# Kernel optimization log

Measured on AMD Instinct MI355X. Metric: run time of the kernel, lower is better.

The kernel has to match this reference:

```python
import jax, jax.numpy as jnp
import numpy as np

N_RF = 25   # contour integration RF extent (must be odd, 7-55)
N_CH = 96   # AlexNet conv1 feature maps


def _get_coaligned_masks(weights_type, rf_len, non_overlapping_rfs=True):
    """Faithful numpy replication of the manually-defined coalignment masks."""
    half_rf = rf_len // 2
    kernel = np.zeros((N_CH, rf_len, rf_len), dtype=np.float32)
    step = 3 if non_overlapping_rfs else 1
    pre = list(range(0, half_rf, step))
    post = list(range(half_rf + step, rf_len, step))
    kernel[10, pre, half_rf] = 1
    kernel[10, post, half_rf] = 1
    if weights_type != 'enhance':
        kernel[10, half_rf, pre] = -1
        kernel[10, half_rf, post] = -1
    kernel[5, half_rf, pre] = 1
    kernel[5, half_rf, post] = 1
    if weights_type != 'enhance':
        kernel[5, pre, half_rf] = -1
        kernel[5, post, half_rf] = -1
    kernel[54, (1, 4, 6, 9, 15, 17, 20, 23), (8, 9, 10, 11, 13, 14, 15, 16)] = 1
    kernel[64, list(range(0, half_rf, 3)), list(range(0, half_rf, 3))] = 1
    kernel[64, list(range(half_rf + 3, rf_len, 3)), list(range(half_rf + 3, rf_len, 3))] = 1
    if weights_type != 'enhance':
        kernel[64, list(range(rf_len - 1, half_rf, -3)), list(range(0, half_rf, 3))] = -1
        kernel[64, list(range(half_rf - 3, -1, -3)), list(range(half_rf + 3, rf_len, 3))] = -1
    kernel[67, :, :] = np.copy(kernel[54, :, :])
    kernel[78, (1, 3, 7, 10, 14, 17, 21, 23), (17, 16, 14, 13, 11, 10, 8, 7)] = 1
    return kernel


def setup_inputs() -> dict:
    key = jax.random.key(0)
    x = jax.random.normal(key, (128, 55, 55, N_CH), dtype=jnp.float32)  # NHWC, AlexNet conv1 output
    kernel = jnp.asarray(_get_coaligned_masks('enhance_and_suppress', N_RF))  # [ch, n, n]
    return {"x": x, "kernel": kernel}


def reference(x, kernel):
    # The per-(i,j) python loop in the original is exactly a per-channel (depthwise)
    # cross-correlation with the fixed mask kernel, SAME padding (n//2 each side),
    # followed by (identity) activation and residual add.
    ch = x.shape[-1]
    k = jnp.transpose(kernel, (1, 2, 0))[:, :, None, :]  # [n, n, 1, ch] HWIO depthwise
    lateral = jax.lax.conv_general_dilated(
        x, k,
        window_strides=(1, 1),
        padding='SAME',
        dimension_numbers=('NHWC', 'HWIO', 'NHWC'),
        feature_group_count=ch,
    )
    # activation is linear (None) -> identity
    return lateral + x
```

## Files before the change

kernel.cpp:

```cpp
#include <hip/hip_runtime.h>

#define NCH   96
#define RF    25
#define HALF  12
#define HW    55
#define PLANE (HW * HW)
#define CAP   32
#define MAXA  6
#define TH    11
#define SROWS (TH + 2*HALF)
#define LDSW  56

#define WS_META_OFF (NCH * 4 + NCH * CAP * 4 * 2)

__global__ void prep_taps(const float* __restrict__ kern, int* __restrict__ counts,
                          int* __restrict__ tap_off, float* __restrict__ tap_w) {
    const int c    = blockIdx.x;
    const int lane = threadIdx.x;
    const float* kc = kern + c * (RF * RF);
    int base = 0;
    for (int seg = 0; seg < RF * RF; seg += 64) {
        const int i = seg + lane;
        const float w = (i < RF * RF) ? kc[i] : 0.0f;
        const unsigned long long m = __ballot(w != 0.0f);
        const int pos = base + __popcll(m & ((1ull << lane) - 1ull));
        if (w != 0.0f && pos < CAP) {
            const int dy = i / RF, dx = i - dy * RF;
            tap_off[c * CAP + pos] = (dy << 8) | dx;
            tap_w[c * CAP + pos]   = w;
        }
        base += __popcll(m);
    }
    if (lane == 0) counts[c] = base;
}

__global__ void prep_meta(const int* __restrict__ counts, int* __restrict__ meta) {
    __shared__ int scnt[NCH];
    if (threadIdx.x < NCH) scnt[threadIdx.x] = counts[threadIdx.x];
    __syncthreads();
    if (threadIdx.x == 0) {
        int na = 0;
        bool fallback = false;
        for (int ch = 0; ch < NCH; ++ch) {
            if (scnt[ch] > 0) {
                if (scnt[ch] > CAP) fallback = true;
                if (na < MAXA) meta[1 + na] = ch;
                ++na;
            }
        }
        if (na > MAXA) fallback = true;
        meta[0] = fallback ? 999 : na;
        for (int a = (na > MAXA ? 0 : na); a < MAXA; ++a) meta[1 + a] = 0;
    }
}

__global__ __launch_bounds__(256, 3) void contour_tile(
        const float* __restrict__ x, const float* __restrict__ kern,
        const int* __restrict__ counts, const int* __restrict__ tap_off,
        const float* __restrict__ tap_w, const int* __restrict__ meta,
        float* __restrict__ out) {
    __shared__ float sh[MAXA][SROWS][LDSW];

    const int b    = blockIdx.x;
    const int xcd  = b & 7;
    const int slot = b >> 3;
    const int imgI = slot / 5;
    const int ty   = slot - imgI * 5;
    const int n    = xcd + (imgI << 3);
    const int y0   = ty * TH;

    const float* xn = x   + (size_t)n * (PLANE * NCH);
    float*       on = out + (size_t)n * (PLANE * NCH);

    const int n_active = meta[0];

    if (n_active <= MAXA) {
        const int tot = n_active * (SROWS * HW);
        for (int idx = threadIdx.x; idx < tot; idx += 256) {
            const int a   = idx / (SROWS * HW);
            const int rem = idx - a * (SROWS * HW);
            const int s   = rem / HW;
            const int col = rem - s * HW;
            const int gy  = y0 - HALF + s;
            float v = 0.0f;
            if ((unsigned)gy < (unsigned)HW)
                v = xn[(size_t)(gy * HW + col) * NCH + meta[1 + a]];
            sh[a][s][col] = v;
        }
        __syncthreads();

        const float4* xs = (const float4*)(xn + (size_t)y0 * HW * NCH);
        float4*       os = (float4*)      (on + (size_t)y0 * HW * NCH);
        const int totc = TH * HW * (NCH / 4);
        for (int idx = threadIdx.x; idx < totc; idx += 256)
            os[idx] = xs[idx];
        __syncthreads();

        const int totb = n_active * (TH * HW);
        for (int idx = threadIdx.x; idx < totb; idx += 256) {
            const int a   = idx / (TH * HW);
            const int rem = idx - a * (TH * HW);
            const int r   = rem / HW;
            const int col = rem - r * HW;
            const int c   = meta[1 + a];
            const int cnt = counts[c];
            float acc = sh[a][r + HALF][col];
            for (int t = 0; t < cnt; ++t) {
                const int off = tap_off[c * CAP + t];
                const float w = tap_w[c * CAP + t];
                const int dy = off >> 8, dx = off & 255;
                const int xx = col + dx - HALF;
                const bool ok = (unsigned)xx < (unsigned)HW;
                const int  xc = min(max(xx, 0), HW - 1);
                const float v = sh[a][r + dy][xc];
                acc += ok ? w * v : 0.0f;
            }
            on[(size_t)((y0 + r) * HW + col) * NCH + c] = acc;
        }
    } else {
        for (int idx = threadIdx.x; idx < TH * HW * (NCH / 4); idx += 256) {
            const int g   = idx % (NCH / 4);
            const int pix = idx / (NCH / 4);
            const int r   = pix / HW;
            const int col = pix - r * HW;
            const int py  = y0 + r;
            const size_t pbase = (size_t)(py * HW + col) * NCH;
            const float4 xv = *(const float4*)(xn + pbase + g * 4);
            float acc[4] = {xv.x, xv.y, xv.z, xv.w};
            for (int kk = 0; kk < 4; ++kk) {
                const int c = g * 4 + kk;
                const int cnt = counts[c];
                if (cnt == 0) continue;
                float a = 0.0f;
                if (cnt <= CAP) {
                    for (int t = 0; t < cnt; ++t) {
                        const int off = tap_off[c * CAP + t];
                        const float w = tap_w[c * CAP + t];
                        const int dy = off >> 8, dx = off & 255;
                        const int yy = py + dy - HALF;
                        const int xx = col + dx - HALF;
                        if ((unsigned)yy < (unsigned)HW && (unsigned)xx < (unsigned)HW)
                            a += w * xn[(size_t)(yy * HW + xx) * NCH + c];
                    }
                } else {
                    for (int dy = 0; dy < RF; ++dy) {
                        for (int dx = 0; dx < RF; ++dx) {
                            const float w = kern[(c * RF + dy) * RF + dx];
                            if (w == 0.0f) continue;
                            const int yy = py + dy - HALF;
                            const int xx = col + dx - HALF;
                            if ((unsigned)yy < (unsigned)HW && (unsigned)xx < (unsigned)HW)
                                a += w * xn[(size_t)(yy * HW + xx) * NCH + c];
                        }
                    }
                }
                acc[kk] += a;
            }
            *(float4*)(on + pbase + g * 4) = make_float4(acc[0], acc[1], acc[2], acc[3]);
        }
    }
}

extern "C" void kernel_launch(void* const* d_in, const int* in_sizes, int n_in,
                              void* d_out, int out_size, void* d_ws, size_t ws_size,
                              hipStream_t stream) {
    const float* x    = (const float*)d_in[0];
    const float* kern = (const float*)d_in[1];
    float* out = (float*)d_out;

    int*   counts  = (int*)d_ws;
    int*   tap_off = (int*)((char*)d_ws + NCH * 4);
    float* tap_w   = (float*)((char*)d_ws + NCH * 4 + NCH * CAP * 4);
    int*   meta    = (int*)((char*)d_ws + WS_META_OFF);

    prep_taps<<<NCH, 64, 0, stream>>>(kern, counts, tap_off, tap_w);
    prep_meta<<<1, 128, 0, stream>>>(counts, meta);

    contour_tile<<<8 * 80, 256, 0, stream>>>(x, kern, counts, tap_off, tap_w, meta, out);
}
```

Baseline: 417.2 us.

## Merge prep kernels, enlarge tiles, and fill LDS interior from the copy pass

Fuses the two setup kernels into one 1024-thread launch. Each contour block now covers a quarter image of 13-14 rows with 1024 threads, giving 512 blocks. While copying the residual through float4 loads, the block scatters the active channels straight into the LDS halo tile, so only the top and bottom halo rows are read separately from global memory. Tap offsets and weights are staged in LDS instead of being reread from global memory. The goal is less halo overfetch, fewer redundant global reads and fewer launches, at the cost of a per-element channel lookup during the copy and larger blocks that may limit occupancy.

```diff
diff --git a/kernel.cpp b/kernel.cpp
--- a/kernel.cpp
+++ b/kernel.cpp
@@ -7,36 +7,35 @@
 #define PLANE (HW * HW)
 #define CAP   32
 #define MAXA  6
-#define TH    11
-#define SROWS (TH + 2*HALF)
+#define SROWS 38
 #define LDSW  56
 
 #define WS_META_OFF (NCH * 4 + NCH * CAP * 4 * 2)
 
-__global__ void prep_taps(const float* __restrict__ kern, int* __restrict__ counts,
-                          int* __restrict__ tap_off, float* __restrict__ tap_w) {
-    const int c    = blockIdx.x;
-    const int lane = threadIdx.x;
-    const float* kc = kern + c * (RF * RF);
-    int base = 0;
-    for (int seg = 0; seg < RF * RF; seg += 64) {
-        const int i = seg + lane;
-        const float w = (i < RF * RF) ? kc[i] : 0.0f;
-        const unsigned long long m = __ballot(w != 0.0f);
-        const int pos = base + __popcll(m & ((1ull << lane) - 1ull));
-        if (w != 0.0f && pos < CAP) {
-            const int dy = i / RF, dx = i - dy * RF;
-            tap_off[c * CAP + pos] = (dy << 8) | dx;
-            tap_w[c * CAP + pos]   = w;
-        }
-        base += __popcll(m);
-    }
-    if (lane == 0) counts[c] = base;
-}
-
-__global__ void prep_meta(const int* __restrict__ counts, int* __restrict__ meta) {
+__global__ __launch_bounds__(1024) void prep_all(
+        const float* __restrict__ kern, int* __restrict__ counts,
+        int* __restrict__ tap_off, float* __restrict__ tap_w,
+        int* __restrict__ meta) {
     __shared__ int scnt[NCH];
-    if (threadIdx.x < NCH) scnt[threadIdx.x] = counts[threadIdx.x];
+    const int wave = threadIdx.x >> 6;
+    const int lane = threadIdx.x & 63;
+    for (int c = wave; c < NCH; c += 16) {
+        const float* kc = kern + c * (RF * RF);
+        int base = 0;
+        for (int seg = 0; seg < RF * RF; seg += 64) {
+            const int i = seg + lane;
+            const float w = (i < RF * RF) ? kc[i] : 0.0f;
+            const unsigned long long m = __ballot(w != 0.0f);
+            const int pos = base + __popcll(m & ((1ull << lane) - 1ull));
+            if (w != 0.0f && pos < CAP) {
+                const int dy = i / RF, dx = i - dy * RF;
+                tap_off[c * CAP + pos] = (dy << 8) | dx;
+                tap_w[c * CAP + pos]   = w;
+            }
+            base += __popcll(m);
+        }
+        if (lane == 0) { counts[c] = base; scnt[c] = base; }
+    }
     __syncthreads();
     if (threadIdx.x == 0) {
         int na = 0;
@@ -54,60 +53,101 @@
     }
 }
 
-__global__ __launch_bounds__(256, 3) void contour_tile(
+__global__ __launch_bounds__(1024, 8) void contour_tile(
         const float* __restrict__ x, const float* __restrict__ kern,
         const int* __restrict__ counts, const int* __restrict__ tap_off,
         const float* __restrict__ tap_w, const int* __restrict__ meta,
         float* __restrict__ out) {
     __shared__ float sh[MAXA][SROWS][LDSW];
-
+    __shared__ float tw[MAXA][CAP];
+    __shared__ int   toff[MAXA][CAP];
+    __shared__ int   tcnt[MAXA];
+    __shared__ int   chA[MAXA];
+    __shared__ signed char c2a[NCH];
+
+    const int tid  = threadIdx.x;
     const int b    = blockIdx.x;
     const int xcd  = b & 7;
-    const int slot = b >> 3;
-    const int imgI = slot / 5;
-    const int ty   = slot - imgI * 5;
-    const int n    = xcd + (imgI << 3);
-    const int y0   = ty * TH;
+    const int s    = b >> 3;
+    const int n    = xcd + ((s >> 2) << 3);
+    const int q    = s & 3;
+    const int y0   = q * 14;
+    const int rows = (q < 3) ? 14 : 13;
+    const int npx  = rows * HW;
 
     const float* xn = x   + (size_t)n * (PLANE * NCH);
     float*       on = out + (size_t)n * (PLANE * NCH);
 
-    const int n_active = meta[0];
-
-    if (n_active <= MAXA) {
-        const int tot = n_active * (SROWS * HW);
-        for (int idx = threadIdx.x; idx < tot; idx += 256) {
-            const int a   = idx / (SROWS * HW);
-            const int rem = idx - a * (SROWS * HW);
-            const int s   = rem / HW;
-            const int col = rem - s * HW;
-            const int gy  = y0 - HALF + s;
+    const int na = meta[0];
+    const bool fast = (na <= MAXA);
+
+    if (tid < NCH) c2a[tid] = -1;
+    __syncthreads();
+    if (fast) {
+        if (tid < MAXA) {
+            const int c = (tid < na) ? meta[1 + tid] : -1;
+            chA[tid]  = c;
+            tcnt[tid] = (c >= 0) ? counts[c] : 0;
+        }
+        if (tid < na) c2a[meta[1 + tid]] = (signed char)tid;
+        if (tid >= 64 && tid < 64 + MAXA * CAP) {
+            const int a = (tid - 64) / CAP, t = (tid - 64) % CAP;
+            const int c = (a < na) ? meta[1 + a] : 0;
+            toff[a][t] = tap_off[c * CAP + t];
+            tw[a][t]   = tap_w[c * CAP + t];
+        }
+    }
+    __syncthreads();
+
+    {
+        const float4* xs = (const float4*)(xn + (size_t)y0 * HW * NCH);
+        float4*       os = (float4*)      (on + (size_t)y0 * HW * NCH);
+        const int totA = npx * (NCH / 4);
+        for (int idx = tid; idx < totA; idx += 1024) {
+            const float4 v = xs[idx];
+            os[idx] = v;
+            if (fast) {
+                const int pixel = idx / 24;
+                const int g     = idx - pixel * 24;
+                const int r     = pixel / HW;
+                const int col   = pixel - r * HW;
+                const float vv[4] = {v.x, v.y, v.z, v.w};
+                #pragma unroll
+                for (int kk = 0; kk < 4; ++kk) {
+                    const int a = c2a[g * 4 + kk];
+                    if (a >= 0) sh[a][r + HALF][col] = vv[kk];
+                }
+            }
+        }
+    }
+
+    if (fast) {
+        const int totB = na * 24 * HW;
+        for (int idx = tid; idx < totB; idx += 1024) {
+            const int a   = idx / (24 * HW);
+            const int rem = idx - a * (24 * HW);
+            const int hs  = rem / HW;
+            const int col = rem - hs * HW;
+            const int sr  = (hs < HALF) ? hs : hs + rows;
+            const int gy  = y0 - HALF + sr;
             float v = 0.0f;
             if ((unsigned)gy < (unsigned)HW)
-                v = xn[(size_t)(gy * HW + col) * NCH + meta[1 + a]];
-            sh[a][s][col] = v;
+                v = xn[(size_t)(gy * HW + col) * NCH + chA[a]];
+            sh[a][sr][col] = v;
         }
         __syncthreads();
 
-        const float4* xs = (const float4*)(xn + (size_t)y0 * HW * NCH);
-        float4*       os = (float4*)      (on + (size_t)y0 * HW * NCH);
-        const int totc = TH * HW * (NCH / 4);
-        for (int idx = threadIdx.x; idx < totc; idx += 256)
-            os[idx] = xs[idx];
-        __syncthreads();
-
-        const int totb = n_active * (TH * HW);
-        for (int idx = threadIdx.x; idx < totb; idx += 256) {
-            const int a   = idx / (TH * HW);
-            const int rem = idx - a * (TH * HW);
+        const int totC = na * npx;
+        for (int idx = tid; idx < totC; idx += 1024) {
+            const int a   = idx / npx;
+            const int rem = idx - a * npx;
             const int r   = rem / HW;
             const int col = rem - r * HW;
-            const int c   = meta[1 + a];
-            const int cnt = counts[c];
+            const int cnt = tcnt[a];
             float acc = sh[a][r + HALF][col];
             for (int t = 0; t < cnt; ++t) {
-                const int off = tap_off[c * CAP + t];
-                const float w = tap_w[c * CAP + t];
+                const int off = toff[a][t];
+                const float w = tw[a][t];
                 const int dy = off >> 8, dx = off & 255;
                 const int xx = col + dx - HALF;
                 const bool ok = (unsigned)xx < (unsigned)HW;
@@ -115,10 +155,10 @@
                 const float v = sh[a][r + dy][xc];
                 acc += ok ? w * v : 0.0f;
             }
-            on[(size_t)((y0 + r) * HW + col) * NCH + c] = acc;
+            on[(size_t)((y0 + r) * HW + col) * NCH + chA[a]] = acc;
         }
     } else {
-        for (int idx = threadIdx.x; idx < TH * HW * (NCH / 4); idx += 256) {
+        for (int idx = tid; idx < npx * (NCH / 4); idx += 1024) {
             const int g   = idx % (NCH / 4);
             const int pix = idx / (NCH / 4);
             const int r   = pix / HW;
@@ -131,7 +171,7 @@
                 const int c = g * 4 + kk;
                 const int cnt = counts[c];
                 if (cnt == 0) continue;
-                float a = 0.0f;
+                float aa = 0.0f;
                 if (cnt <= CAP) {
                     for (int t = 0; t < cnt; ++t) {
                         const int off = tap_off[c * CAP + t];
@@ -140,21 +180,20 @@
                         const int yy = py + dy - HALF;
                         const int xx = col + dx - HALF;
                         if ((unsigned)yy < (unsigned)HW && (unsigned)xx < (unsigned)HW)
-                            a += w * xn[(size_t)(yy * HW + xx) * NCH + c];
+                            aa += w * xn[(size_t)(yy * HW + xx) * NCH + c];
                     }
                 } else {
-                    for (int dy = 0; dy < RF; ++dy) {
+                    for (int dy = 0; dy < RF; ++dy)
                         for (int dx = 0; dx < RF; ++dx) {
                             const float w = kern[(c * RF + dy) * RF + dx];
                             if (w == 0.0f) continue;
                             const int yy = py + dy - HALF;
                             const int xx = col + dx - HALF;
                             if ((unsigned)yy < (unsigned)HW && (unsigned)xx < (unsigned)HW)
-                                a += w * xn[(size_t)(yy * HW + xx) * NCH + c];
+                                aa += w * xn[(size_t)(yy * HW + xx) * NCH + c];
                         }
-                    }
                 }
-                acc[kk] += a;
+                acc[kk] += aa;
             }
             *(float4*)(on + pbase + g * 4) = make_float4(acc[0], acc[1], acc[2], acc[3]);
         }
@@ -173,8 +212,7 @@
     float* tap_w   = (float*)((char*)d_ws + NCH * 4 + NCH * CAP * 4);
     int*   meta    = (int*)((char*)d_ws + WS_META_OFF);
 
-    prep_taps<<<NCH, 64, 0, stream>>>(kern, counts, tap_off, tap_w);
-    prep_meta<<<1, 128, 0, stream>>>(counts, meta);
-
-    contour_tile<<<8 * 80, 256, 0, stream>>>(x, kern, counts, tap_off, tap_w, meta, out);
+    prep_all<<<1, 1024, 0, stream>>>(kern, counts, tap_off, tap_w, meta);
+
+    contour_tile<<<512, 1024, 0, stream>>>(x, kern, counts, tap_off, tap_w, meta, out);
 }
```

After: 382.2 us. 1.09x faster.
